# Optimization experiments

Hardware: AMD Instinct MI355X
Metric: run time of the kernel (lower is better)

Reference implementation:

```python
import jax, jax.numpy as jnp
import numpy as np

B, S, D, H = 4, 2048, 1024, 16
HD = D // H  # 64


def setup_inputs() -> dict:
    key = jax.random.key(0)
    ks = jax.random.split(key, 4)
    scale = 0.02
    return {
        "hidden_states": jax.random.normal(ks[0], (B, S, D), dtype=jnp.float32),
        "pad": jnp.ones((B, S), dtype=jnp.float32),  # 1 = keep, 0 = pad
        "wq": jax.random.normal(ks[1], (D, D), dtype=jnp.float32) * scale,
        "bq": jnp.zeros((D,), dtype=jnp.float32),
        "wk": jax.random.normal(ks[2], (D, D), dtype=jnp.float32) * scale,
        "bk": jnp.zeros((D,), dtype=jnp.float32),
        "wv": jax.random.normal(ks[3], (D, D), dtype=jnp.float32) * scale,
        "bv": jnp.zeros((D,), dtype=jnp.float32),
    }


def reference(hidden_states, pad, wq, bq, wk, bk, wv, bv):
    # QKV projections (torch Linear: x @ W^T + b); weights stored as [out, in]
    q = hidden_states @ wq.T + bq  # [B,S,D]
    k = hidden_states @ wk.T + bk
    v = hidden_states @ wv.T + bv

    def split_heads(x):
        return x.reshape(B, S, H, HD).transpose(0, 2, 1, 3)  # [B,H,S,HD]

    q, k, v = split_heads(q), split_heads(k), split_heads(v)

    score = jnp.einsum("bhqd,bhkd->bhqk", q, k) / jnp.sqrt(jnp.float32(HD))
    # additive pad mask: (1 - pad) * -1e9, broadcast over heads and query dim
    mask_bias = (1.0 - pad)[:, None, None, :] * (-1e9)
    prob = jax.nn.softmax(score + mask_bias, axis=-1)  # [B,H,S,S]

    context = jnp.einsum("bhqk,bhkd->bhqd", prob, v)  # [B,H,S,HD]
    context = context.transpose(0, 2, 1, 3).reshape(B, S, D)
    return context
```

## Files before the change

### kernel.cpp

```cpp
#include <hip/hip_runtime.h>
#include <cstdint>
#include <cstddef>

#define B_ 4
#define S_ 2048
#define D_ 1024
#define H_ 16

typedef unsigned short u16;
typedef unsigned int u32;
typedef __attribute__((ext_vector_type(8))) short bf16x8;
typedef __attribute__((ext_vector_type(4))) float f32x4;

__device__ __forceinline__ u32 cvtpk_bf16(float lo, float hi) {
  u32 r;
  asm("v_cvt_pk_bf16_f32 %0, %1, %2" : "=v"(r) : "v"(lo), "v"(hi));
  return r;
}

__device__ __forceinline__ u16 f2bf1(float v) {
  return (u16)cvtpk_bf16(v, v);
}

__device__ __forceinline__ float exp2raw(float x) {
  float r;
  asm("v_exp_f32 %0, %1" : "=v"(r) : "v"(x));
  return r;
}

__device__ __forceinline__ float max3f(float a, float b, float c) {
  return fmaxf(fmaxf(a, b), c);
}

__device__ __forceinline__ f32x4 mfma16(bf16x8 a, bf16x8 b, f32x4 c) {
  return __builtin_amdgcn_mfma_f32_16x16x32_bf16(a, b, c, 0, 0, 0);
}

__device__ __forceinline__ void gload_lds16(const u16* g, u16* l) {
  __builtin_amdgcn_global_load_lds((const __attribute__((address_space(1))) void*)g,
                                   (__attribute__((address_space(3))) void*)l,
                                   16, 0, 0);
}

__global__ __launch_bounds__(256) void cvt_kernel(const float4* __restrict__ src,
                                                  uint2* __restrict__ dst, int n4) {
  int i = blockIdx.x * 256 + threadIdx.x;
  if (i < n4) {
    float4 v = src[i];
    uint2 o;
    o.x = cvtpk_bf16(v.x, v.y);
    o.y = cvtpk_bf16(v.z, v.w);
    dst[i] = o;
  }
}

__global__ __launch_bounds__(256) void qkv_gemm(
    const u16* __restrict__ A, const u16* __restrict__ Bm,
    const float* __restrict__ bq, const float* __restrict__ bk,
    const float* __restrict__ bv,
    u16* __restrict__ qbuf, u16* __restrict__ kbuf, u16* __restrict__ vtbuf)
{
  __shared__ __align__(16) u16 lA[128 * 64];
  __shared__ __align__(16) u16 lB[128 * 64];

  const int bid = blockIdx.x;
  const int wg = ((bid & 7) * 192) + (bid >> 3);
  const int bm = wg & 63;
  const int bn = wg >> 6;
  const int tid = threadIdx.x;
  const int wid = tid >> 6, lane = tid & 63;
  const int g = lane >> 4, c = lane & 15;
  const int wm = wid & 1, wn = wid >> 1;
  const int lrow = lane >> 3;
  const int lcb = (lane & 7) ^ lrow;

  f32x4 acc[4][4];
#pragma unroll
  for (int i = 0; i < 4; ++i)
#pragma unroll
    for (int j = 0; j < 4; ++j) acc[i][j] = (f32x4)0.0f;

  const u16* Ab = A + (size_t)(bm * 128) * 1024;
  const u16* Bb = Bm + (size_t)(bn * 128) * 1024;

  for (int kt = 0; kt < 16; ++kt) {
    const int k0 = kt * 64;
#pragma unroll
    for (int jj = 0; jj < 4; ++jj) {
      const int r0 = wid * 32 + jj * 8;
      gload_lds16(Ab + (size_t)(r0 + lrow) * 1024 + k0 + lcb * 8, lA + r0 * 64);
      gload_lds16(Bb + (size_t)(r0 + lrow) * 1024 + k0 + lcb * 8, lB + r0 * 64);
    }
    __syncthreads();
#pragma unroll
    for (int ks = 0; ks < 2; ++ks) {
      bf16x8 af[4], bfv[4];
#pragma unroll
      for (int mi = 0; mi < 4; ++mi) {
        const int row = wm * 64 + mi * 16 + c;
        const int cb = (ks * 4 + g) ^ (c & 7);
        af[mi] = *(const bf16x8*)(lA + row * 64 + cb * 8);
      }
#pragma unroll
      for (int ni = 0; ni < 4; ++ni) {
        const int row = wn * 64 + ni * 16 + c;
        const int cb = (ks * 4 + g) ^ (c & 7);
        bfv[ni] = *(const bf16x8*)(lB + row * 64 + cb * 8);
      }
#pragma unroll
      for (int mi = 0; mi < 4; ++mi)
#pragma unroll
        for (int ni = 0; ni < 4; ++ni)
          acc[mi][ni] = mfma16(af[mi], bfv[ni], acc[mi][ni]);
    }
    __syncthreads();
  }

  const int m0 = bm * 128 + wm * 64;
  const int n0 = bn * 128 + wn * 64;
#pragma unroll
  for (int ni = 0; ni < 4; ++ni) {
    const int col = n0 + ni * 16 + c;
    const int which = col >> 10;
    const int d = col & 1023;
    const int hh = d >> 6, hd = d & 63;
    const float* bp = (which == 0) ? bq : (which == 1) ? bk : bv;
    const float bias = bp[d];
#pragma unroll
    for (int mi = 0; mi < 4; ++mi) {
      const int row0 = m0 + mi * 16 + g * 4;
      const int bb = row0 >> 11, s0 = row0 & 2047;
      if (which == 2) {
        uint2 pv;
        pv.x = cvtpk_bf16(acc[mi][ni][0] + bias, acc[mi][ni][1] + bias);
        pv.y = cvtpk_bf16(acc[mi][ni][2] + bias, acc[mi][ni][3] + bias);
        *(uint2*)&vtbuf[((size_t)(bb * 16 + hh) * 64 + hd) * 2048 + s0] = pv;
      } else {
        u16* dst = (which == 0) ? qbuf : kbuf;
        const float sc = (which == 0) ? 0.125f : 1.0f;
#pragma unroll
        for (int r = 0; r < 4; ++r) {
          dst[((size_t)(bb * 16 + hh) * 2048 + (s0 + r)) * 64 + hd] =
              f2bf1((acc[mi][ni][r] + bias) * sc);
        }
      }
    }
  }
}

__global__ __launch_bounds__(256) void attn_kernel(
    const u16* __restrict__ qbuf, const u16* __restrict__ kbuf,
    const u16* __restrict__ vtbuf, const float* __restrict__ pad,
    float* __restrict__ out)
{
  __shared__ __align__(16) u16 lK[64 * 64];
  __shared__ __align__(16) u16 lV[64 * 64];
  __shared__ __align__(16) u16 lP[4 * 32 * 64];
  __shared__ __align__(16) float lMask[64];

  const int bid = blockIdx.x;
  const int wg = ((bid & 7) << 7) | (bid >> 3);
  const int bh = wg >> 4;
  const int qb = wg & 15;
  const int b = bh >> 4;
  const int h = bh & 15;
  const int tid = threadIdx.x;
  const int wid = tid >> 6, lane = tid & 63;
  const int g = lane >> 4, c = lane & 15;
  const int q0 = qb * 128 + wid * 32;

  const u16* qp = qbuf + (size_t)bh * S_ * 64;
  const u16* kp = kbuf + (size_t)bh * S_ * 64;
  const u16* vp = vtbuf + (size_t)bh * 64 * S_;

  bf16x8 qf[2][2];
#pragma unroll
  for (int nt = 0; nt < 2; ++nt)
#pragma unroll
    for (int ks = 0; ks < 2; ++ks)
      qf[nt][ks] = *(const bf16x8*)(qp + (size_t)(q0 + nt * 16 + c) * 64 + ks * 32 + g * 8);

  f32x4 o[2][4];
#pragma unroll
  for (int mi = 0; mi < 2; ++mi)
#pragma unroll
    for (int nh = 0; nh < 4; ++nh) o[mi][nh] = (f32x4)0.0f;

  float mst[2] = {-3e38f, -3e38f};
  float lst[2] = {0.0f, 0.0f};

  const int lrow = lane >> 3;
  const int lcb = (lane & 7) ^ lrow;
  u16* lPw = lP + wid * (32 * 64);
  const float LOG2E = 1.44269504f;

  for (int j = 0; j < 32; ++j) {
    const int kv0 = j * 64;
#pragma unroll
    for (int jj = 0; jj < 2; ++jj) {
      const int r0 = wid * 16 + jj * 8;
      gload_lds16(kp + (size_t)(kv0 + r0 + lrow) * 64 + lcb * 8, lK + r0 * 64);
      gload_lds16(vp + (size_t)(r0 + lrow) * 2048 + kv0 + lcb * 8, lV + r0 * 64);
    }
    if (tid < 64) lMask[tid] = (1.0f - pad[b * S_ + kv0 + tid]) * (-1e9f);
    __syncthreads();

    f32x4 st[4][2];
#pragma unroll
    for (int mt = 0; mt < 4; ++mt) { st[mt][0] = (f32x4)0.0f; st[mt][1] = (f32x4)0.0f; }
#pragma unroll
    for (int ks = 0; ks < 2; ++ks) {
#pragma unroll
      for (int mt = 0; mt < 4; ++mt) {
        const int row = mt * 16 + c;
        const int cb = (ks * 4 + g) ^ (c & 7);
        const bf16x8 kf = *(const bf16x8*)(lK + row * 64 + cb * 8);
        st[mt][0] = mfma16(kf, qf[0][ks], st[mt][0]);
        st[mt][1] = mfma16(kf, qf[1][ks], st[mt][1]);
      }
    }

    const bool mhit = !__all(lMask[lane] == 0.0f);
    float mb[4][4];
    if (mhit) {
#pragma unroll
      for (int mt = 0; mt < 4; ++mt) {
        const float4 m4 = *(const float4*)&lMask[mt * 16 + g * 4];
        mb[mt][0] = m4.x; mb[mt][1] = m4.y; mb[mt][2] = m4.z; mb[mt][3] = m4.w;
      }
    }

#pragma unroll
    for (int nt = 0; nt < 2; ++nt) {
      if (mhit) {
#pragma unroll
        for (int mt = 0; mt < 4; ++mt)
#pragma unroll
          for (int r = 0; r < 4; ++r) st[mt][nt][r] += mb[mt][r];
      }
      float tmax = max3f(st[0][nt][0], st[0][nt][1], st[0][nt][2]);
      tmax = max3f(tmax, st[0][nt][3], st[1][nt][0]);
      tmax = max3f(tmax, st[1][nt][1], st[1][nt][2]);
      tmax = max3f(tmax, st[1][nt][3], st[2][nt][0]);
      tmax = max3f(tmax, st[2][nt][1], st[2][nt][2]);
      tmax = max3f(tmax, st[2][nt][3], st[3][nt][0]);
      tmax = max3f(tmax, st[3][nt][1], st[3][nt][2]);
      tmax = fmaxf(tmax, st[3][nt][3]);
      tmax = fmaxf(tmax, __shfl_xor(tmax, 16));
      tmax = fmaxf(tmax, __shfl_xor(tmax, 32));

      if (!__all(tmax - mst[nt] <= 8.0f)) {
        const float mnew = fmaxf(mst[nt], tmax);
        const float fac = exp2raw((mst[nt] - mnew) * LOG2E);
        mst[nt] = mnew;
        lst[nt] *= fac;
#pragma unroll
        for (int r = 0; r < 4; ++r) {
          const float fr = __shfl(fac, g * 4 + r);
#pragma unroll
          for (int nh = 0; nh < 4; ++nh) o[nt][nh][r] *= fr;
        }
      }

      const float ml = mst[nt] * LOG2E;
      float rsum = 0.0f;
#pragma unroll
      for (int mt = 0; mt < 4; ++mt)
#pragma unroll
        for (int r = 0; r < 4; ++r) {
          const float p = exp2raw(fmaf(st[mt][nt][r], LOG2E, -ml));
          st[mt][nt][r] = p;
          rsum += p;
        }
      rsum += __shfl_xor(rsum, 16);
      rsum += __shfl_xor(rsum, 32);
      lst[nt] += rsum;

#pragma unroll
      for (int mt = 0; mt < 4; ++mt) {
        uint2 pk;
        pk.x = cvtpk_bf16(st[mt][nt][0], st[mt][nt][1]);
        pk.y = cvtpk_bf16(st[mt][nt][2], st[mt][nt][3]);
        const int rowq = nt * 16 + c;
        const int cb = (2 * mt + (g >> 1)) ^ (c & 7);
        *(uint2*)(lPw + rowq * 64 + cb * 8 + (g & 1) * 4) = pk;
      }
    }

#pragma unroll
    for (int ks = 0; ks < 2; ++ks) {
      bf16x8 pa[2];
#pragma unroll
      for (int mi = 0; mi < 2; ++mi) {
        const int row = mi * 16 + c;
        const int cb = (ks * 4 + g) ^ (c & 7);
        pa[mi] = *(const bf16x8*)(lPw + row * 64 + cb * 8);
      }
#pragma unroll
      for (int nh = 0; nh < 4; ++nh) {
        const int row = nh * 16 + c;
        const int cb = (ks * 4 + g) ^ (c & 7);
        const bf16x8 vf = *(const bf16x8*)(lV + row * 64 + cb * 8);
#pragma unroll
        for (int mi = 0; mi < 2; ++mi)
          o[mi][nh] = mfma16(pa[mi], vf, o[mi][nh]);
      }
    }
    __syncthreads();
  }

#pragma unroll
  for (int mi = 0; mi < 2; ++mi) {
#pragma unroll
    for (int r = 0; r < 4; ++r) {
      const float lr = __shfl(lst[mi], g * 4 + r);
      const float inv = 1.0f / lr;
      const int srow = q0 + mi * 16 + g * 4 + r;
      float* op = out + (size_t)(b * S_ + srow) * D_ + h * 64;
#pragma unroll
      for (int nh = 0; nh < 4; ++nh)
        op[nh * 16 + c] = o[mi][nh][r] * inv;
    }
  }
}

extern "C" void kernel_launch(void* const* d_in, const int* in_sizes, int n_in,
                              void* d_out, int out_size, void* d_ws, size_t ws_size,
                              hipStream_t stream) {
  const float* hs  = (const float*)d_in[0];
  const float* pad = (const float*)d_in[1];
  const float* wq  = (const float*)d_in[2];
  const float* bq  = (const float*)d_in[3];
  const float* wk  = (const float*)d_in[4];
  const float* bk  = (const float*)d_in[5];
  const float* wv  = (const float*)d_in[6];
  const float* bv  = (const float*)d_in[7];
  float* out = (float*)d_out;

  char* ws = (char*)d_ws;
  u16* Abf   = (u16*)ws;
  u16* Bbf   = (u16*)(ws + (16u << 20));
  u16* qbuf  = (u16*)(ws + (22u << 20));
  u16* kbuf  = (u16*)(ws + (38u << 20));
  u16* vtbuf = (u16*)(ws + (54u << 20));

  cvt_kernel<<<8192, 256, 0, stream>>>((const float4*)hs, (uint2*)Abf, 2097152);
  cvt_kernel<<<1024, 256, 0, stream>>>((const float4*)wq, (uint2*)Bbf, 262144);
  cvt_kernel<<<1024, 256, 0, stream>>>((const float4*)wk, (uint2*)(Bbf + (1u << 20)), 262144);
  cvt_kernel<<<1024, 256, 0, stream>>>((const float4*)wv, (uint2*)(Bbf + (2u << 20)), 262144);

  qkv_gemm<<<1536, 256, 0, stream>>>(Abf, Bbf, bq, bk, bv, qbuf, kbuf, vtbuf);
  attn_kernel<<<1024, 256, 0, stream>>>(qbuf, kbuf, vtbuf, pad, out);
}
```

Measured before the change: 313.2 us.

## Double-buffer K/V tiles, preload pad mask, compute row sums via MFMA

Adds a second LDS buffer for K and V so the next tile's global-to-LDS loads are issued before computing on the current tile, leaving one barrier per iteration. The whole pad mask for the batch row is converted once into LDS at kernel start instead of per tile. Softmax row sums now come from an MFMA of the bf16 probabilities against a ones vector, replacing the scalar sum and cross-lane shuffles. s_setprio brackets the MFMA sections. The cost is more LDS (an extra 16KB for the buffers plus 8KB for the mask), which may lower occupancy, and row sums taken from bf16-rounded probabilities.

```diff
diff --git a/kernel.cpp b/kernel.cpp
--- a/kernel.cpp
+++ b/kernel.cpp
@@ -153,10 +153,10 @@
     const u16* __restrict__ vtbuf, const float* __restrict__ pad,
     float* __restrict__ out)
 {
-  __shared__ __align__(16) u16 lK[64 * 64];
-  __shared__ __align__(16) u16 lV[64 * 64];
+  __shared__ __align__(16) u16 lK[2][64 * 64];
+  __shared__ __align__(16) u16 lV[2][64 * 64];
   __shared__ __align__(16) u16 lP[4 * 32 * 64];
-  __shared__ __align__(16) float lMask[64];
+  __shared__ __align__(16) float lMaskAll[2048];
 
   const int bid = blockIdx.x;
   const int wg = ((bid & 7) << 7) | (bid >> 3);
@@ -173,6 +173,19 @@
   const u16* kp = kbuf + (size_t)bh * S_ * 64;
   const u16* vp = vtbuf + (size_t)bh * 64 * S_;
 
+  {
+    const float4* p4 = (const float4*)(pad + (size_t)b * S_);
+#pragma unroll
+    for (int i = 0; i < 2; ++i) {
+      const int idx = tid + i * 256;
+      const float4 v = p4[idx];
+      float4 m;
+      m.x = (1.0f - v.x) * (-1e9f); m.y = (1.0f - v.y) * (-1e9f);
+      m.z = (1.0f - v.z) * (-1e9f); m.w = (1.0f - v.w) * (-1e9f);
+      *(float4*)&lMaskAll[idx * 4] = m;
+    }
+  }
+
   bf16x8 qf[2][2];
 #pragma unroll
   for (int nt = 0; nt < 2; ++nt)
@@ -185,47 +198,60 @@
   for (int mi = 0; mi < 2; ++mi)
 #pragma unroll
     for (int nh = 0; nh < 4; ++nh) o[mi][nh] = (f32x4)0.0f;
-
+  f32x4 lsum[2];
+  lsum[0] = (f32x4)0.0f; lsum[1] = (f32x4)0.0f;
   float mst[2] = {-3e38f, -3e38f};
-  float lst[2] = {0.0f, 0.0f};
 
   const int lrow = lane >> 3;
   const int lcb = (lane & 7) ^ lrow;
   u16* lPw = lP + wid * (32 * 64);
   const float LOG2E = 1.44269504f;
 
+  const short one_bf = (short)0x3F80;
+  const bf16x8 vones = {one_bf, one_bf, one_bf, one_bf, one_bf, one_bf, one_bf, one_bf};
+
+  auto stageKV = [&](int jt, int bufn) {
+    const int kv0 = jt * 64;
+#pragma unroll
+    for (int jj = 0; jj < 2; ++jj) {
+      const int r0 = wid * 16 + jj * 8;
+      gload_lds16(kp + (size_t)(kv0 + r0 + lrow) * 64 + lcb * 8, &lK[bufn][r0 * 64]);
+      gload_lds16(vp + (size_t)(r0 + lrow) * 2048 + kv0 + lcb * 8, &lV[bufn][r0 * 64]);
+    }
+  };
+
+  stageKV(0, 0);
+  asm volatile("s_waitcnt vmcnt(0)" ::: "memory");
+  __syncthreads();
+
+  int cur = 0;
   for (int j = 0; j < 32; ++j) {
     const int kv0 = j * 64;
-#pragma unroll
-    for (int jj = 0; jj < 2; ++jj) {
-      const int r0 = wid * 16 + jj * 8;
-      gload_lds16(kp + (size_t)(kv0 + r0 + lrow) * 64 + lcb * 8, lK + r0 * 64);
-      gload_lds16(vp + (size_t)(r0 + lrow) * 2048 + kv0 + lcb * 8, lV + r0 * 64);
-    }
-    if (tid < 64) lMask[tid] = (1.0f - pad[b * S_ + kv0 + tid]) * (-1e9f);
-    __syncthreads();
+    if (j < 31) stageKV(j + 1, cur ^ 1);
 
     f32x4 st[4][2];
 #pragma unroll
     for (int mt = 0; mt < 4; ++mt) { st[mt][0] = (f32x4)0.0f; st[mt][1] = (f32x4)0.0f; }
+    __builtin_amdgcn_s_setprio(1);
 #pragma unroll
     for (int ks = 0; ks < 2; ++ks) {
 #pragma unroll
       for (int mt = 0; mt < 4; ++mt) {
         const int row = mt * 16 + c;
         const int cb = (ks * 4 + g) ^ (c & 7);
-        const bf16x8 kf = *(const bf16x8*)(lK + row * 64 + cb * 8);
+        const bf16x8 kf = *(const bf16x8*)(&lK[cur][row * 64 + cb * 8]);
         st[mt][0] = mfma16(kf, qf[0][ks], st[mt][0]);
         st[mt][1] = mfma16(kf, qf[1][ks], st[mt][1]);
       }
     }
-
-    const bool mhit = !__all(lMask[lane] == 0.0f);
+    __builtin_amdgcn_s_setprio(0);
+
+    const bool mhit = !__all(lMaskAll[kv0 + lane] == 0.0f);
     float mb[4][4];
     if (mhit) {
 #pragma unroll
       for (int mt = 0; mt < 4; ++mt) {
-        const float4 m4 = *(const float4*)&lMask[mt * 16 + g * 4];
+        const float4 m4 = *(const float4*)&lMaskAll[kv0 + mt * 16 + g * 4];
         mb[mt][0] = m4.x; mb[mt][1] = m4.y; mb[mt][2] = m4.z; mb[mt][3] = m4.w;
       }
     }
@@ -253,28 +279,21 @@
         const float mnew = fmaxf(mst[nt], tmax);
         const float fac = exp2raw((mst[nt] - mnew) * LOG2E);
         mst[nt] = mnew;
-        lst[nt] *= fac;
 #pragma unroll
         for (int r = 0; r < 4; ++r) {
           const float fr = __shfl(fac, g * 4 + r);
+          lsum[nt][r] *= fr;
 #pragma unroll
           for (int nh = 0; nh < 4; ++nh) o[nt][nh][r] *= fr;
         }
       }
 
       const float ml = mst[nt] * LOG2E;
-      float rsum = 0.0f;
 #pragma unroll
       for (int mt = 0; mt < 4; ++mt)
 #pragma unroll
-        for (int r = 0; r < 4; ++r) {
-          const float p = exp2raw(fmaf(st[mt][nt][r], LOG2E, -ml));
-          st[mt][nt][r] = p;
-          rsum += p;
-        }
-      rsum += __shfl_xor(rsum, 16);
-      rsum += __shfl_xor(rsum, 32);
-      lst[nt] += rsum;
+        for (int r = 0; r < 4; ++r)
+          st[mt][nt][r] = exp2raw(fmaf(st[mt][nt][r], LOG2E, -ml));
 
 #pragma unroll
       for (int mt = 0; mt < 4; ++mt) {
@@ -287,6 +306,7 @@
       }
     }
 
+    __builtin_amdgcn_s_setprio(1);
 #pragma unroll
     for (int ks = 0; ks < 2; ++ks) {
       bf16x8 pa[2];
@@ -296,25 +316,30 @@
         const int cb = (ks * 4 + g) ^ (c & 7);
         pa[mi] = *(const bf16x8*)(lPw + row * 64 + cb * 8);
       }
+      lsum[0] = mfma16(pa[0], vones, lsum[0]);
+      lsum[1] = mfma16(pa[1], vones, lsum[1]);
 #pragma unroll
       for (int nh = 0; nh < 4; ++nh) {
         const int row = nh * 16 + c;
         const int cb = (ks * 4 + g) ^ (c & 7);
-        const bf16x8 vf = *(const bf16x8*)(lV + row * 64 + cb * 8);
+        const bf16x8 vf = *(const bf16x8*)(&lV[cur][row * 64 + cb * 8]);
 #pragma unroll
         for (int mi = 0; mi < 2; ++mi)
           o[mi][nh] = mfma16(pa[mi], vf, o[mi][nh]);
       }
     }
+    __builtin_amdgcn_s_setprio(0);
+
+    asm volatile("s_waitcnt vmcnt(0)" ::: "memory");
     __syncthreads();
+    cur ^= 1;
   }
 
 #pragma unroll
   for (int mi = 0; mi < 2; ++mi) {
 #pragma unroll
     for (int r = 0; r < 4; ++r) {
-      const float lr = __shfl(lst[mi], g * 4 + r);
-      const float inv = 1.0f / lr;
+      const float inv = 1.0f / lsum[mi][r];
       const int srow = q0 + mi * 16 + g * 4 + r;
       float* op = out + (size_t)(b * S_ + srow) * D_ + h * 64;
 #pragma unroll
```

Result: faster. 304.3 us (-2.8%).
